# Kernel optimization log

Hardware: AMD Instinct MI355X
Metric: run time of the kernel (lower is better)

The kernel has to match this reference:

```python
import jax, jax.numpy as jnp
import numpy as np
import math

NUM_HEADS = 12
POS_BND = 16                 # patch_num
RPE_NUM = 2 * POS_BND + 1    # 33
LOGIT_SCALE_MAX = math.log(1.0 / 0.01)
EPS_NORM = 1e-12


def setup_inputs() -> dict:
    key = jax.random.key(0)
    ks = jax.random.split(key, 8)
    L, N, C = 257, 32, 768   # L = 16*16 patches + 1 CLS
    H, W = 16, 16
    x = jax.random.normal(ks[0], (L, N, C), dtype=jnp.float32)
    depth = jax.random.uniform(ks[1], (N, 1, H, W), dtype=jnp.float32)
    in_proj_w = jax.random.normal(ks[2], (3 * C, C), dtype=jnp.float32) * 0.02
    in_proj_b = jnp.zeros((3 * C,), dtype=jnp.float32)
    out_proj_w = jax.random.normal(ks[3], (C, C), dtype=jnp.float32) * 0.02
    out_proj_b = jnp.zeros((C,), dtype=jnp.float32)
    rpe_table = jax.random.normal(ks[4], (3 * RPE_NUM, NUM_HEADS), dtype=jnp.float32) * 0.02
    logit_scale = jnp.log(10.0) * jnp.ones((NUM_HEADS, 1, 1), dtype=jnp.float32)
    return {
        "x": x, "depth": depth,
        "in_proj_w": in_proj_w, "in_proj_b": in_proj_b,
        "out_proj_w": out_proj_w, "out_proj_b": out_proj_b,
        "rpe_table": rpe_table, "logit_scale": logit_scale,
    }


def _rpe_bias(depth, rpe_table):
    # depth: (B, 1, H, W) -> bias (B*num_heads, H*W, H*W)
    d = depth[:, 0]                              # (B, H, W)
    B, H, W = d.shape
    ii, jj = jnp.meshgrid(jnp.arange(H), jnp.arange(W), indexing="ij")
    xg = (jj.astype(jnp.float32) / (W - 1))[None].repeat(B, axis=0)   # (B,H,W)
    yg = (ii.astype(jnp.float32) / (H - 1))[None].repeat(B, axis=0)
    z_min = d.min(axis=(-2, -1), keepdims=True)
    z_max = d.max(axis=(-2, -1), keepdims=True)
    z = (d - z_min) / (z_max - z_min + 1e-8)
    coords = jnp.stack([xg, yg, z], axis=-1).reshape(B, H * W, 3)     # (B,HW,3)
    rel = coords[:, :, None, :] - coords[:, None, :, :]               # (B,HW,HW,3)
    idx = jnp.clip(jnp.round(rel * POS_BND).astype(jnp.int32), -POS_BND, POS_BND)
    idx = idx + POS_BND + jnp.arange(3, dtype=jnp.int32) * RPE_NUM    # (B,HW,HW,3)
    bias = rpe_table[idx].sum(axis=3)                                 # (B,HW,HW,heads)
    bias = bias.transpose(0, 3, 1, 2)                                 # (B,heads,HW,HW)
    return bias.reshape(-1, H * W, H * W)


def reference(x, depth, in_proj_w, in_proj_b, out_proj_w, out_proj_b, rpe_table, logit_scale):
    L, N, C = x.shape
    Hn = NUM_HEADS
    hd = C // Hn
    qkv = x @ in_proj_w.T + in_proj_b                     # (L,N,3C)
    q, k, v = jnp.split(qkv, 3, axis=-1)
    def to_heads(t):
        return t.reshape(L, N * Hn, hd).transpose(1, 0, 2)  # (N*Hn, L, hd)
    q, k, v = to_heads(q), to_heads(k), to_heads(v)
    # scaled-cosine attention: normalized q,k then clamped exp(log-scale)
    qn = q / jnp.maximum(jnp.linalg.norm(q, axis=-1, keepdims=True), EPS_NORM)
    kn = k / jnp.maximum(jnp.linalg.norm(k, axis=-1, keepdims=True), EPS_NORM)
    attn = jnp.einsum("bld,bmd->blm", qn, kn)             # (N*Hn, L, L)
    scale = jnp.exp(jnp.minimum(logit_scale, LOGIT_SCALE_MAX))   # (Hn,1,1)
    attn = (attn.reshape(N, Hn, L, L) * scale).reshape(N * Hn, L, L)
    # relative-position bias on patch tokens (skip CLS at index 0)
    res = _rpe_bias(depth, rpe_table)                     # (N*Hn, L-1, L-1)
    attn = attn.at[:, 1:, 1:].add(res)
    attn = jax.nn.softmax(attn, axis=-1)
    out = jnp.einsum("blm,bmd->bld", attn, v)             # (N*Hn, L, hd)
    out = out.transpose(1, 0, 2).reshape(L, N, C)
    out = out @ out_proj_w.T + out_proj_b
    return out, attn
```

## Files before the change

kernel.cpp:

```cpp
#include <hip/hip_runtime.h>
#include <math.h>

#define L_TOK 257
#define N_B 32
#define C_DIM 768
#define N_H 12
#define HD 64
#define BH (N_B * N_H)
#define M_TOK (L_TOK * N_B)
#define HW 256
#define RPE_NUM 33
#define LOGIT_MAX 4.6051701859880913680f
#define VT_STRIDE 264
#define MT_Q 65
#define NT_Q 18
#define NT_O 6
#define NTK 24

typedef unsigned short ushort;
typedef unsigned int uint;
typedef __attribute__((ext_vector_type(8))) short short8;
typedef __attribute__((ext_vector_type(4))) float f32x4;

__device__ __forceinline__ ushort f2bf_rn(float f) {
  uint u = __float_as_uint(f);
  uint r = (u + 0x7FFF + ((u >> 16) & 1)) >> 16;
  return (ushort)r;
}
__device__ __forceinline__ float bf2f(ushort h) {
  return __uint_as_float(((uint)h) << 16);
}

__device__ __forceinline__ int xcd_swz(int wid, int nwg) {
  int q = nwg >> 3, r = nwg & 7;
  int xcd = wid & 7, pos = wid >> 3;
  int base = (xcd < r) ? xcd * (q + 1) : r * (q + 1) + (xcd - r) * q;
  return base + pos;
}

__device__ __forceinline__ void tile_map(int bid, int MT, int NT, int nwg,
                                         int& m0, int& nt) {
  int wid = xcd_swz(bid, nwg);
  int per = 8 * NT;
  int s = wid / per;
  int rem = wid - s * per;
  int msz = MT - s * 8; if (msz > 8) msz = 8;
  int mi = rem % msz, ni = rem / msz;
  m0 = (s * 8 + mi) * 128;
  nt = ni;
}

__global__ __launch_bounds__(256)
void cvt_split(const float* __restrict__ src, ushort* __restrict__ hi,
               ushort* __restrict__ lo, int n) {
  int i = (blockIdx.x * 256 + threadIdx.x) * 4;
  if (i + 3 >= n + 3) return;
  if (i + 3 < n) {
    float4 v = *(const float4*)(src + i);
    ushort h0 = f2bf_rn(v.x), h1 = f2bf_rn(v.y), h2 = f2bf_rn(v.z), h3 = f2bf_rn(v.w);
    ushort l0 = f2bf_rn(v.x - bf2f(h0)), l1 = f2bf_rn(v.y - bf2f(h1));
    ushort l2 = f2bf_rn(v.z - bf2f(h2)), l3 = f2bf_rn(v.w - bf2f(h3));
    *(ushort4*)(hi + i) = make_ushort4(h0, h1, h2, h3);
    *(ushort4*)(lo + i) = make_ushort4(l0, l1, l2, l3);
  } else {
    for (int k = i; k < n; ++k) {
      float vv = src[k];
      ushort h = f2bf_rn(vv);
      hi[k] = h; lo[k] = f2bf_rn(vv - bf2f(h));
    }
  }
}

__device__ __forceinline__ void stage_pair(const ushort* g0, const ushort* g1,
                                           ushort* l, uint so) {
  __builtin_amdgcn_global_load_lds(
      (const __attribute__((address_space(1))) void*)g0,
      (__attribute__((address_space(3))) void*)((char*)l + so), 16, 0, 0);
  __builtin_amdgcn_global_load_lds(
      (const __attribute__((address_space(1))) void*)g1,
      (__attribute__((address_space(3))) void*)((char*)l + so + 4096), 16, 0, 0);
}

#define PH_WAIT(N)                                        \
  asm volatile("s_waitcnt vmcnt(" #N ")" ::: "memory");   \
  __builtin_amdgcn_s_barrier();                           \
  __builtin_amdgcn_sched_barrier(0);

#define PH_LGKM()                                         \
  asm volatile("s_waitcnt lgkmcnt(0)" ::: "memory");      \
  __builtin_amdgcn_sched_barrier(0);

__device__ __forceinline__ void gemm3_core(
    const ushort* __restrict__ Ahi, const ushort* __restrict__ Alo,
    const ushort* __restrict__ Bhi, const ushort* __restrict__ Blo,
    int m0, int n0, ushort* lds, f32x4 (&acc)[4][4]) {
  const int K = C_DIM, M = M_TOK;
  const int t = threadIdx.x;
  const int wave = t >> 6, lane = t & 63;
  const int wm = (wave & 1) * 64, wn = (wave >> 1) * 64;
  const int frm = lane & 15, fs = lane >> 4;
  const int sx = (fs ^ ((frm >> 1) & 3)) * 8;

  const int ar = t >> 2;
  const int acs = ((t & 3) ^ ((ar >> 1) & 3)) * 8;
  const uint so = (uint)(t & 192) * 16;

  int rA0 = m0 + ar;      if (rA0 > M - 1) rA0 = M - 1;
  int rA1 = m0 + 64 + ar; if (rA1 > M - 1) rA1 = M - 1;
  const size_t gA0 = (size_t)rA0 * K + acs;
  const size_t gA1 = (size_t)rA1 * K + acs;
  const size_t gB0 = (size_t)(n0 + ar) * K + acs;
  const size_t gB1 = (size_t)(n0 + 64 + ar) * K + acs;

  stage_pair(Ahi + gA0, Ahi + gA1, lds, so);
  stage_pair(Bhi + gB0, Bhi + gB1, lds + 4096, so);
  stage_pair(Alo + gA0, Alo + gA1, lds + 8192, so);
  stage_pair(Blo + gB0, Blo + gB1, lds + 12288, so);

  short8 ah[4], bh[4], al[4], bl[4];

#pragma unroll 2
  for (int kt = 0; kt < NTK - 1; ++kt) {
    const int curo = (kt & 1) << 14;
    const int nxo = curo ^ 16384;
    const int kn = (kt + 1) * 32;
    PH_WAIT(4)
#pragma unroll
    for (int i = 0; i < 4; ++i) {
      ah[i] = *(const short8*)(lds + curo + (wm + i * 16 + frm) * 32 + sx);
      bh[i] = *(const short8*)(lds + curo + 4096 + (wn + i * 16 + frm) * 32 + sx);
    }
    stage_pair(Ahi + gA0 + kn, Ahi + gA1 + kn, lds + nxo, so);
    stage_pair(Bhi + gB0 + kn, Bhi + gB1 + kn, lds + nxo + 4096, so);
    PH_LGKM()
    __builtin_amdgcn_s_setprio(1);
#pragma unroll
    for (int i = 0; i < 4; ++i)
#pragma unroll
      for (int j = 0; j < 4; ++j)
        acc[i][j] = __builtin_amdgcn_mfma_f32_16x16x32_bf16(ah[i], bh[j], acc[i][j], 0, 0, 0);
    __builtin_amdgcn_s_setprio(0);
    __builtin_amdgcn_sched_barrier(0);
    PH_WAIT(4)
#pragma unroll
    for (int i = 0; i < 4; ++i) {
      al[i] = *(const short8*)(lds + curo + 8192 + (wm + i * 16 + frm) * 32 + sx);
      bl[i] = *(const short8*)(lds + curo + 12288 + (wn + i * 16 + frm) * 32 + sx);
    }
    stage_pair(Alo + gA0 + kn, Alo + gA1 + kn, lds + nxo + 8192, so);
    stage_pair(Blo + gB0 + kn, Blo + gB1 + kn, lds + nxo + 12288, so);
    PH_LGKM()
    __builtin_amdgcn_s_setprio(1);
#pragma unroll
    for (int i = 0; i < 4; ++i)
#pragma unroll
      for (int j = 0; j < 4; ++j)
        acc[i][j] = __builtin_amdgcn_mfma_f32_16x16x32_bf16(al[i], bh[j], acc[i][j], 0, 0, 0);
#pragma unroll
    for (int i = 0; i < 4; ++i)
#pragma unroll
      for (int j = 0; j < 4; ++j)
        acc[i][j] = __builtin_amdgcn_mfma_f32_16x16x32_bf16(ah[i], bl[j], acc[i][j], 0, 0, 0);
    __builtin_amdgcn_s_setprio(0);
    __builtin_amdgcn_sched_barrier(0);
  }
  {
    const int curo = ((NTK - 1) & 1) << 14;
    PH_WAIT(4)
#pragma unroll
    for (int i = 0; i < 4; ++i) {
      ah[i] = *(const short8*)(lds + curo + (wm + i * 16 + frm) * 32 + sx);
      bh[i] = *(const short8*)(lds + curo + 4096 + (wn + i * 16 + frm) * 32 + sx);
    }
    PH_LGKM()
#pragma unroll
    for (int i = 0; i < 4; ++i)
#pragma unroll
      for (int j = 0; j < 4; ++j)
        acc[i][j] = __builtin_amdgcn_mfma_f32_16x16x32_bf16(ah[i], bh[j], acc[i][j], 0, 0, 0);
    __builtin_amdgcn_sched_barrier(0);
    PH_WAIT(0)
#pragma unroll
    for (int i = 0; i < 4; ++i) {
      al[i] = *(const short8*)(lds + curo + 8192 + (wm + i * 16 + frm) * 32 + sx);
      bl[i] = *(const short8*)(lds + curo + 12288 + (wn + i * 16 + frm) * 32 + sx);
    }
    PH_LGKM()
#pragma unroll
    for (int i = 0; i < 4; ++i)
#pragma unroll
      for (int j = 0; j < 4; ++j)
        acc[i][j] = __builtin_amdgcn_mfma_f32_16x16x32_bf16(al[i], bh[j], acc[i][j], 0, 0, 0);
#pragma unroll
    for (int i = 0; i < 4; ++i)
#pragma unroll
      for (int j = 0; j < 4; ++j)
        acc[i][j] = __builtin_amdgcn_mfma_f32_16x16x32_bf16(ah[i], bl[j], acc[i][j], 0, 0, 0);
    __builtin_amdgcn_sched_barrier(0);
  }
}

__global__ __launch_bounds__(256, 2)
void gemm_qkv_fused(const ushort* __restrict__ Ahi, const ushort* __restrict__ Alo,
                    const ushort* __restrict__ Bhi, const ushort* __restrict__ Blo,
                    const float* __restrict__ bias,
                    ushort* __restrict__ qhi, ushort* __restrict__ qlo,
                    ushort* __restrict__ khi, ushort* __restrict__ klo,
                    float* __restrict__ vout) {
  __shared__ __align__(16) ushort lds[32768];
  int m0, nt;
  tile_map(blockIdx.x, MT_Q, NT_Q, MT_Q * NT_Q, m0, nt);
  const int n0 = nt * 128;
  f32x4 acc[4][4] = {};
  gemm3_core(Ahi, Alo, Bhi, Blo, m0, n0, lds, acc);

  const int M = M_TOK;
  const int t = threadIdx.x;
  const int wave = t >> 6, lane = t & 63;
  const int wm = (wave & 1) * 64, wn = (wave >> 1) * 64;
  const int c0 = lane & 15, g = lane >> 4;
  const int colBase = n0 + wn;
  const int sect = colBase / C_DIM;
  const int hh = (colBase - sect * C_DIM) >> 6;
  float bv[4];
#pragma unroll
  for (int j = 0; j < 4; ++j) bv[j] = bias[colBase + j * 16 + c0];

#pragma unroll
  for (int i = 0; i < 4; ++i) {
#pragma unroll
    for (int r = 0; r < 4; ++r) {
      const int row = m0 + wm + i * 16 + g * 4 + r;
      float lv[4];
#pragma unroll
      for (int j = 0; j < 4; ++j) lv[j] = acc[i][j][r] + bv[j];
      if (sect == 2) {
        if (row < M) {
          int l = row >> 5, n = row & 31;
          size_t ob = ((size_t)((n * N_H + hh) * L_TOK + l)) * HD;
#pragma unroll
          for (int j = 0; j < 4; ++j) vout[ob + j * 16 + c0] = lv[j];
        }
      } else {
        float ss = lv[0] * lv[0] + lv[1] * lv[1] + lv[2] * lv[2] + lv[3] * lv[3];
        ss += __shfl_xor(ss, 1);
        ss += __shfl_xor(ss, 2);
        ss += __shfl_xor(ss, 4);
        ss += __shfl_xor(ss, 8);
        float inv = 1.0f / fmaxf(sqrtf(ss), 1e-12f);
        if (row < M) {
          int l = row >> 5, n = row & 31;
          size_t ob = ((size_t)((n * N_H + hh) * L_TOK + l)) * HD;
          ushort* dh = sect ? khi : qhi;
          ushort* dl = sect ? klo : qlo;
#pragma unroll
          for (int j = 0; j < 4; ++j) {
            float val = lv[j] * inv;
            ushort hv = f2bf_rn(val);
            dh[ob + j * 16 + c0] = hv;
            dl[ob + j * 16 + c0] = f2bf_rn(val - bf2f(hv));
          }
        }
      }
    }
  }
}

__global__ __launch_bounds__(256, 2)
void gemm_out(const ushort* __restrict__ Ahi, const ushort* __restrict__ Alo,
              const ushort* __restrict__ Bhi, const ushort* __restrict__ Blo,
              const float* __restrict__ bias, float* __restrict__ Cout) {
  __shared__ __align__(16) ushort lds[32768];
  int m0, nt;
  tile_map(blockIdx.x, MT_Q, NT_O, MT_Q * NT_O, m0, nt);
  const int n0 = nt * 128;
  f32x4 acc[4][4] = {};
  gemm3_core(Ahi, Alo, Bhi, Blo, m0, n0, lds, acc);

  const int M = M_TOK, Nn = C_DIM;
  const int t = threadIdx.x;
  const int wave = t >> 6, lane = t & 63;
  const int wm = (wave & 1) * 64, wn = (wave >> 1) * 64;
  const int ecol = lane & 15;
#pragma unroll
  for (int j = 0; j < 4; ++j) {
    int col = n0 + wn + j * 16 + ecol;
    float bv = bias[col];
#pragma unroll
    for (int i = 0; i < 4; ++i) {
      int rbase = m0 + wm + i * 16 + (lane >> 4) * 4;
#pragma unroll
      for (int r = 0; r < 4; ++r) {
        int row = rbase + r;
        if (row < M) Cout[(size_t)row * Nn + col] = acc[i][j][r] + bv;
      }
    }
  }
}

__global__ __launch_bounds__(256)
void vt_make(const float* __restrict__ v, ushort* __restrict__ vthi,
             ushort* __restrict__ vtlo) {
  __shared__ float sT[64][65];
  const int b = blockIdx.x;
  const int t = threadIdx.x;
  const float* vb = v + (size_t)b * L_TOK * HD;
  ushort* vh = vthi + (size_t)b * HD * VT_STRIDE;
  ushort* vl = vtlo + (size_t)b * HD * VT_STRIDE;
  for (int k0 = 0; k0 < 256; k0 += 64) {
#pragma unroll
    for (int p = 0; p < 16; ++p) {
      int idx = p * 256 + t;
      int k = idx >> 6, d = idx & 63;
      sT[d][k] = vb[(size_t)(k0 + k) * HD + d];
    }
    __syncthreads();
#pragma unroll
    for (int p = 0; p < 16; ++p) {
      int idx = p * 256 + t;
      int d = idx >> 6, k = idx & 63;
      float val = sT[d][k];
      ushort h = f2bf_rn(val);
      vh[(size_t)d * VT_STRIDE + k0 + k] = h;
      vl[(size_t)d * VT_STRIDE + k0 + k] = f2bf_rn(val - bf2f(h));
    }
    __syncthreads();
  }
  if (t < HD) {
    float val = vb[(size_t)256 * HD + t];
    ushort h = f2bf_rn(val);
    vh[(size_t)t * VT_STRIDE + 256] = h;
    vl[(size_t)t * VT_STRIDE + 256] = f2bf_rn(val - bf2f(h));
  }
}

__global__ __launch_bounds__(256)
void attn_mfma(const ushort* __restrict__ qhi, const ushort* __restrict__ qlo,
               const ushort* __restrict__ khi, const ushort* __restrict__ klo,
               const float* __restrict__ depth, const float* __restrict__ rpe,
               const float* __restrict__ lscale, float* __restrict__ P) {
  __shared__ __align__(16) ushort sKh[256 * 72];
  __shared__ __align__(16) ushort sKl[256 * 72];
  __shared__ float cz_s[HW];
  __shared__ float txd[32], tyd[32], tzt[36];
  __shared__ float red_s[16];
  __shared__ float s256[4][16];
  __shared__ float qs[HD];
  __shared__ float lg6_sh;

  const int tile = blockIdx.x;
  const int b = blockIdx.y;
  const int n = b / N_H, h = b - n * N_H;
  const int t = threadIdx.x;
  const int lane = t & 63, wave = t >> 6;

  float dval = depth[n * HW + t];
  float mn = dval, mx = dval;
#pragma unroll
  for (int o = 32; o > 0; o >>= 1) {
    mn = fminf(mn, __shfl_down(mn, o));
    mx = fmaxf(mx, __shfl_down(mx, o));
  }
  if (lane == 0) { red_s[wave] = mn; red_s[8 + wave] = mx; }
  __syncthreads();
  float zmin = fminf(fminf(red_s[0], red_s[1]), fminf(red_s[2], red_s[3]));
  float zmax = fmaxf(fmaxf(red_s[8], red_s[9]), fmaxf(red_s[10], red_s[11]));
  float den = zmax - zmin + 1e-8f;
  cz_s[t] = (dval - zmin) / den;
  if (t < 31) {
    int d = t - 15;
    int ix = (int)rintf((float)d * (16.0f / 15.0f));
    ix = max(-16, min(16, ix));
    txd[t] = rpe[(ix + 16) * N_H + h];
    tyd[t] = rpe[(RPE_NUM + ix + 16) * N_H + h];
  }
  if (t < RPE_NUM) tzt[t] = rpe[(2 * RPE_NUM + t) * N_H + h];
  const float scale = expf(fminf(lscale[h], LOGIT_MAX));

  const ushort* khb = khi + (size_t)b * L_TOK * HD;
  const ushort* klb = klo + (size_t)b * L_TOK * HD;
#pragma unroll
  for (int it = 0; it < 8; ++it) {
    int idx = it * 256 + t;
    int j = idx >> 3, c = (idx & 7) * 8;
    *(uint4*)(sKh + j * 72 + c) = *(const uint4*)(khb + (size_t)j * HD + c);
    *(uint4*)(sKl + j * 72 + c) = *(const uint4*)(klb + (size_t)j * HD + c);
  }
  __syncthreads();

  const int qrow = tile * 64 + 16 * wave;
  const size_t qoff = ((size_t)b * L_TOK + qrow + (lane & 15)) * HD + (lane >> 4) * 8;
  short8 qh0 = *(const short8*)(qhi + qoff);
  short8 qh1 = *(const short8*)(qhi + qoff + 32);
  short8 ql0 = *(const short8*)(qlo + qoff);
  short8 ql1 = *(const short8*)(qlo + qoff + 32);

  f32x4 acc[16] = {};
#pragma unroll
  for (int jt = 0; jt < 16; ++jt) {
    const ushort* bp = sKh + (jt * 16 + (lane & 15)) * 72 + (lane >> 4) * 8;
    const ushort* bq = sKl + (jt * 16 + (lane & 15)) * 72 + (lane >> 4) * 8;
    short8 bh0 = *(const short8*)(bp);
    short8 bh1 = *(const short8*)(bp + 32);
    short8 bl0 = *(const short8*)(bq);
    short8 bl1 = *(const short8*)(bq + 32);
    acc[jt] = __builtin_amdgcn_mfma_f32_16x16x32_bf16(qh0, bh0, acc[jt], 0, 0, 0);
    acc[jt] = __builtin_amdgcn_mfma_f32_16x16x32_bf16(qh1, bh1, acc[jt], 0, 0, 0);
    acc[jt] = __builtin_amdgcn_mfma_f32_16x16x32_bf16(qh0, bl0, acc[jt], 0, 0, 0);
    acc[jt] = __builtin_amdgcn_mfma_f32_16x16x32_bf16(qh1, bl1, acc[jt], 0, 0, 0);
    acc[jt] = __builtin_amdgcn_mfma_f32_16x16x32_bf16(ql0, bh0, acc[jt], 0, 0, 0);
    acc[jt] = __builtin_amdgcn_mfma_f32_16x16x32_bf16(ql1, bh1, acc[jt], 0, 0, 0);
  }

  {
    const ushort* k6h = khb + (size_t)256 * HD + (lane >> 4) * 8;
    const ushort* k6l = klb + (size_t)256 * HD + (lane >> 4) * 8;
    float p = 0.f;
#pragma unroll
    for (int j = 0; j < 8; ++j) {
      float kf0 = bf2f(k6h[j]) + bf2f(k6l[j]);
      float kf1 = bf2f(k6h[32 + j]) + bf2f(k6l[32 + j]);
      float qf0 = bf2f((ushort)qh0[j]) + bf2f((ushort)ql0[j]);
      float qf1 = bf2f((ushort)qh1[j]) + bf2f((ushort)ql1[j]);
      p = fmaf(qf0, kf0, fmaf(qf1, kf1, p));
    }
    p += __shfl_xor(p, 16);
    p += __shfl_xor(p, 32);
    if (lane < 16) s256[wave][lane] = p;
  }

  const int g = lane >> 4, c0 = lane & 15;

  float lg6[4];
#pragma unroll
  for (int r = 0; r < 4; ++r) {
    int gi = tile * 64 + 16 * wave + 4 * g + r;
    float d6 = s256[wave][4 * g + r];
    float bz = 0.f;
    if (gi >= 1) {
      int dx = ((gi - 1) & 15) - 15;
      int dy = ((gi - 1) >> 4) - 15;
      float rz = (cz_s[gi - 1] - cz_s[255]) * 16.0f;
      int iz = (int)rintf(rz); iz = max(-16, min(16, iz));
      bz = txd[dx + 15] + tyd[dy + 15] + tzt[iz + 16];
    }
    lg6[r] = scale * d6 + bz;
  }

#pragma unroll
  for (int jt = 0; jt < 16; ++jt) {
    int col = jt * 16 + c0;
#pragma unroll
    for (int r = 0; r < 4; ++r) {
      int gi = tile * 64 + 16 * wave + 4 * g + r;
      float lv = scale * acc[jt][r];
      if (col >= 1 && gi >= 1) {
        int dx = ((gi - 1) & 15) - ((col - 1) & 15);
        int dy = ((gi - 1) >> 4) - ((col - 1) >> 4);
        float rz = (cz_s[gi - 1] - cz_s[col - 1]) * 16.0f;
        int iz = (int)rintf(rz); iz = max(-16, min(16, iz));
        lv += txd[dx + 15] + tyd[dy + 15] + tzt[iz + 16];
      }
      acc[jt][r] = lv;
    }
  }

  float* Pb_ = P + (size_t)b * L_TOK * L_TOK;
#pragma unroll
  for (int r = 0; r < 4; ++r) {
    int gi = tile * 64 + 16 * wave + 4 * g + r;
    float m = acc[0][r];
#pragma unroll
    for (int jt = 1; jt < 16; ++jt) m = fmaxf(m, acc[jt][r]);
#pragma unroll
    for (int o = 1; o < 16; o <<= 1) m = fmaxf(m, __shfl_xor(m, o));
    m = fmaxf(m, lg6[r]);
    float s = 0.f;
#pragma unroll
    for (int jt = 0; jt < 16; ++jt) {
      float e = __expf(acc[jt][r] - m);
      acc[jt][r] = e;
      s += e;
    }
#pragma unroll
    for (int o = 1; o < 16; o <<= 1) s += __shfl_xor(s, o);
    float e6 = __expf(lg6[r] - m);
    float inv = 1.0f / (s + e6);
    float* Prow = Pb_ + (size_t)gi * L_TOK;
#pragma unroll
    for (int jt = 0; jt < 16; ++jt)
      Prow[jt * 16 + c0] = acc[jt][r] * inv;
    if (c0 == 0) Prow[256] = e6 * inv;
  }

  if (tile == 0) {
    __syncthreads();
    const size_t q6 = ((size_t)b * L_TOK + 256) * HD;
    if (t < HD) qs[t] = bf2f(qhi[q6 + t]) + bf2f(qlo[q6 + t]);
    __syncthreads();

    const ushort* krh = sKh + t * 72;
    const ushort* krl = sKl + t * 72;
    float dot = 0.f;
#pragma unroll
    for (int c = 0; c < HD; c += 8) {
      ushort4 hv0 = *(const ushort4*)(krh + c);
      ushort4 hv1 = *(const ushort4*)(krh + c + 4);
      ushort4 lv0 = *(const ushort4*)(krl + c);
      ushort4 lv1 = *(const ushort4*)(krl + c + 4);
      dot = fmaf(bf2f(hv0.x) + bf2f(lv0.x), qs[c + 0], dot);
      dot = fmaf(bf2f(hv0.y) + bf2f(lv0.y), qs[c + 1], dot);
      dot = fmaf(bf2f(hv0.z) + bf2f(lv0.z), qs[c + 2], dot);
      dot = fmaf(bf2f(hv0.w) + bf2f(lv0.w), qs[c + 3], dot);
      dot = fmaf(bf2f(hv1.x) + bf2f(lv1.x), qs[c + 4], dot);
      dot = fmaf(bf2f(hv1.y) + bf2f(lv1.y), qs[c + 5], dot);
      dot = fmaf(bf2f(hv1.z) + bf2f(lv1.z), qs[c + 6], dot);
      dot = fmaf(bf2f(hv1.w) + bf2f(lv1.w), qs[c + 7], dot);
    }

    float lg;
    {
      float bsum = 0.f;
      if (t >= 1) {
        int dx = 15 - ((t - 1) & 15);
        int dy = 15 - ((t - 1) >> 4);
        float rz = (cz_s[255] - cz_s[t - 1]) * 16.0f;
        int iz = (int)rintf(rz); iz = max(-16, min(16, iz));
        bsum = txd[dx + 15] + tyd[dy + 15] + tzt[iz + 16];
      }
      lg = scale * dot + bsum;
    }

    if (wave == 0) {
      const ushort* k6h = khi + q6;
      const ushort* k6l = klo + q6;
      float pp = (bf2f(k6h[lane]) + bf2f(k6l[lane])) * qs[lane];
#pragma unroll
      for (int o = 32; o > 0; o >>= 1) pp += __shfl_down(pp, o);
      if (lane == 0) {
        float bz = txd[15] + tyd[15] + tzt[16];
        lg6_sh = scale * pp + bz;
      }
    }

    float m = lg;
#pragma unroll
    for (int o = 32; o > 0; o >>= 1) m = fmaxf(m, __shfl_down(m, o));
    if (lane == 0) red_s[wave] = m;
    __syncthreads();
    float M = fmaxf(fmaxf(red_s[0], red_s[1]), fmaxf(red_s[2], red_s[3]));
    M = fmaxf(M, lg6_sh);
    float e = __expf(lg - M);
    float s = e;
#pragma unroll
    for (int o = 32; o > 0; o >>= 1) s += __shfl_down(s, o);
    if (lane == 0) red_s[8 + wave] = s;
    __syncthreads();
    float e6 = __expf(lg6_sh - M);
    float S = (red_s[8] + red_s[9]) + (red_s[10] + red_s[11]) + e6;
    float inv = 1.0f / S;
    float* Prow = Pb_ + (size_t)256 * L_TOK;
    Prow[t] = e * inv;
    if (t == 0) Prow[256] = e6 * inv;
  }
}

__global__ __launch_bounds__(256)
void pv_mfma(const float* __restrict__ P, const ushort* __restrict__ vthi,
             const ushort* __restrict__ vtlo, const float* __restrict__ v,
             ushort* __restrict__ ahi, ushort* __restrict__ alo) {
  const int b = blockIdx.y;
  const int n = b / N_H, h = b - n * N_H;
  const int t = threadIdx.x;
  const int lane = t & 63, wave = t >> 6;
  const int rbase = blockIdx.x * 128 + wave * 32;
  const float* Pb = P + (size_t)b * L_TOK * L_TOK;
  const ushort* vh = vthi + (size_t)b * HD * VT_STRIDE;
  const ushort* vl = vtlo + (size_t)b * HD * VT_STRIDE;

  const int fm = lane & 15, fk = (lane >> 4) * 8;
  f32x4 acc[2][4] = {};

  for (int k0 = 0; k0 < 256; k0 += 32) {
    short8 ah[2], al[2], bh[4], bl[4];
#pragma unroll
    for (int i = 0; i < 2; ++i) {
      const float* pr = Pb + (size_t)(rbase + i * 16 + fm) * L_TOK + k0 + fk;
#pragma unroll
      for (int j = 0; j < 8; ++j) {
        float pv_ = pr[j];
        ushort hh = f2bf_rn(pv_);
        ah[i][j] = (short)hh;
        al[i][j] = (short)f2bf_rn(pv_ - bf2f(hh));
      }
    }
#pragma unroll
    for (int j = 0; j < 4; ++j) {
      const ushort* bp = vh + (size_t)(j * 16 + fm) * VT_STRIDE + k0 + fk;
      const ushort* bq = vl + (size_t)(j * 16 + fm) * VT_STRIDE + k0 + fk;
      bh[j] = *(const short8*)bp;
      bl[j] = *(const short8*)bq;
    }
#pragma unroll
    for (int i = 0; i < 2; ++i)
#pragma unroll
      for (int j = 0; j < 4; ++j) {
        acc[i][j] = __builtin_amdgcn_mfma_f32_16x16x32_bf16(ah[i], bh[j], acc[i][j], 0, 0, 0);
        acc[i][j] = __builtin_amdgcn_mfma_f32_16x16x32_bf16(ah[i], bl[j], acc[i][j], 0, 0, 0);
        acc[i][j] = __builtin_amdgcn_mfma_f32_16x16x32_bf16(al[i], bh[j], acc[i][j], 0, 0, 0);
        acc[i][j] = __builtin_amdgcn_mfma_f32_16x16x32_bf16(al[i], bl[j], acc[i][j], 0, 0, 0);
      }
  }

  const int g = lane >> 4;
  float v6[4];
#pragma unroll
  for (int j = 0; j < 4; ++j)
    v6[j] = v[((size_t)b * L_TOK + 256) * HD + j * 16 + fm];
#pragma unroll
  for (int i = 0; i < 2; ++i)
#pragma unroll
    for (int r = 0; r < 4; ++r) {
      int row = rbase + i * 16 + g * 4 + r;
      float p6 = Pb[(size_t)row * L_TOK + 256];
#pragma unroll
      for (int j = 0; j < 4; ++j) acc[i][j][r] += p6 * v6[j];
    }

#pragma unroll
  for (int i = 0; i < 2; ++i)
#pragma unroll
    for (int r = 0; r < 4; ++r) {
      int row = rbase + i * 16 + g * 4 + r;
      size_t o = ((size_t)row * N_B + n) * C_DIM + h * HD;
#pragma unroll
      for (int j = 0; j < 4; ++j) {
        float val = acc[i][j][r];
        ushort hv = f2bf_rn(val);
        ahi[o + j * 16 + fm] = hv;
        alo[o + j * 16 + fm] = f2bf_rn(val - bf2f(hv));
      }
    }

  if (blockIdx.x == 0 && t < HD) {
    const float* Prow = Pb + (size_t)256 * L_TOK;
    const float* vb = v + (size_t)b * L_TOK * HD;
    float sum = 0.f;
    for (int k = 0; k < L_TOK; ++k)
      sum = fmaf(Prow[k], vb[(size_t)k * HD + t], sum);
    size_t o = ((size_t)256 * N_B + n) * C_DIM + h * HD + t;
    ushort hv = f2bf_rn(sum);
    ahi[o] = hv;
    alo[o] = f2bf_rn(sum - bf2f(hv));
  }
}

extern "C" void kernel_launch(void* const* d_in, const int* in_sizes, int n_in,
                              void* d_out, int out_size, void* d_ws, size_t ws_size,
                              hipStream_t stream) {
  const float* x      = (const float*)d_in[0];
  const float* depth  = (const float*)d_in[1];
  const float* w_in   = (const float*)d_in[2];
  const float* b_in   = (const float*)d_in[3];
  const float* w_out  = (const float*)d_in[4];
  const float* b_out  = (const float*)d_in[5];
  const float* rpe    = (const float*)d_in[6];
  const float* lscale = (const float*)d_in[7];
  float* out = (float*)d_out;
  float* ws = (float*)d_ws;

  ushort* xhi  = (ushort*)ws;
  ushort* xlo  = xhi + 6316032;
  ushort* vthi = (ushort*)(ws + 6316032);
  ushort* vtlo = vthi + 6488064;
  float*  v    = ws + 18948096;
  ushort* qhi  = (ushort*)(ws + 25264128);
  ushort* qlo  = qhi + 6316032;
  ushort* khi  = qlo + 6316032;
  ushort* klo  = khi + 6316032;
  ushort* wihi = (ushort*)(ws + 37896192);
  ushort* wilo = wihi + 1769472;
  ushort* wohi = wilo + 1769472;
  ushort* wolo = wohi + 589824;
  ushort* ahi  = xhi;
  ushort* alo  = xlo;
  float* Pout = out + 6316032;

  cvt_split<<<6168, 256, 0, stream>>>(x, xhi, xlo, 6316032);
  cvt_split<<<1728, 256, 0, stream>>>(w_in, wihi, wilo, 1769472);
  cvt_split<<<576, 256, 0, stream>>>(w_out, wohi, wolo, 589824);

  gemm_qkv_fused<<<MT_Q * NT_Q, 256, 0, stream>>>(xhi, xlo, wihi, wilo, b_in,
                                                  qhi, qlo, khi, klo, v);
  vt_make<<<BH, 256, 0, stream>>>(v, vthi, vtlo);
  attn_mfma<<<dim3(4, BH), 256, 0, stream>>>(qhi, qlo, khi, klo, depth, rpe, lscale, Pout);
  pv_mfma<<<dim3(2, BH), 256, 0, stream>>>(Pout, vthi, vtlo, v, ahi, alo);

  gemm_out<<<MT_Q * NT_O, 256, 0, stream>>>(ahi, alo, wohi, wolo, b_out, out);
}
```

Measured before the change: 445.9 us.

## Fuse PV matmul into attention kernel using LDS-staged split-bf16 probabilities

Merges the separate pv_mfma kernel into the attention kernel. Each block writes its normalized probability tile as hi/lo bf16 pairs into shared memory, reusing the K buffer, then multiplies it against V^T with MFMA. This avoids re-reading the full fp32 probability matrix from global memory and removes one kernel launch. In exchange it adds a barrier, extra LDS writes and V loads per attention block, and the CLS-row path now reads K from global memory.

```diff
diff --git a/kernel.cpp b/kernel.cpp
--- a/kernel.cpp
+++ b/kernel.cpp
@@ -16,6 +16,7 @@
 #define NT_Q 18
 #define NT_O 6
 #define NTK 24
+#define P_STRIDE 264
 
 typedef unsigned short ushort;
 typedef unsigned int uint;
@@ -335,18 +336,26 @@
 }
 
 __global__ __launch_bounds__(256)
-void attn_mfma(const ushort* __restrict__ qhi, const ushort* __restrict__ qlo,
-               const ushort* __restrict__ khi, const ushort* __restrict__ klo,
-               const float* __restrict__ depth, const float* __restrict__ rpe,
-               const float* __restrict__ lscale, float* __restrict__ P) {
-  __shared__ __align__(16) ushort sKh[256 * 72];
-  __shared__ __align__(16) ushort sKl[256 * 72];
+void attn_pv(const ushort* __restrict__ qhi, const ushort* __restrict__ qlo,
+             const ushort* __restrict__ khi, const ushort* __restrict__ klo,
+             const ushort* __restrict__ vthi, const ushort* __restrict__ vtlo,
+             const float* __restrict__ v,
+             const float* __restrict__ depth, const float* __restrict__ rpe,
+             const float* __restrict__ lscale, float* __restrict__ P,
+             ushort* __restrict__ ahi, ushort* __restrict__ alo) {
+  __shared__ __align__(16) ushort sK[2 * 256 * 72];
   __shared__ float cz_s[HW];
   __shared__ float txd[32], tyd[32], tzt[36];
   __shared__ float red_s[16];
   __shared__ float s256[4][16];
   __shared__ float qs[HD];
   __shared__ float lg6_sh;
+  __shared__ float prow_s[257];
+
+  ushort* sKh = sK;
+  ushort* sKl = sK + 256 * 72;
+  ushort* Psh = sK;
+  ushort* Psl = sK + 64 * P_STRIDE;
 
   const int tile = blockIdx.x;
   const int b = blockIdx.y;
@@ -429,6 +438,8 @@
     if (lane < 16) s256[wave][lane] = p;
   }
 
+  __syncthreads();
+
   const int g = lane >> 4, c0 = lane & 15;
 
   float lg6[4];
@@ -466,9 +477,11 @@
   }
 
   float* Pb_ = P + (size_t)b * L_TOK * L_TOK;
+  float p6v[4];
 #pragma unroll
   for (int r = 0; r < 4; ++r) {
     int gi = tile * 64 + 16 * wave + 4 * g + r;
+    int lrw = 16 * wave + 4 * g + r;
     float m = acc[0][r];
 #pragma unroll
     for (int jt = 1; jt < 16; ++jt) m = fmaxf(m, acc[jt][r]);
@@ -486,21 +499,67 @@
     for (int o = 1; o < 16; o <<= 1) s += __shfl_xor(s, o);
     float e6 = __expf(lg6[r] - m);
     float inv = 1.0f / (s + e6);
+    p6v[r] = e6 * inv;
     float* Prow = Pb_ + (size_t)gi * L_TOK;
 #pragma unroll
-    for (int jt = 0; jt < 16; ++jt)
-      Prow[jt * 16 + c0] = acc[jt][r] * inv;
-    if (c0 == 0) Prow[256] = e6 * inv;
+    for (int jt = 0; jt < 16; ++jt) {
+      float pv_ = acc[jt][r] * inv;
+      Prow[jt * 16 + c0] = pv_;
+      ushort hv = f2bf_rn(pv_);
+      Psh[lrw * P_STRIDE + jt * 16 + c0] = hv;
+      Psl[lrw * P_STRIDE + jt * 16 + c0] = f2bf_rn(pv_ - bf2f(hv));
+    }
+    if (c0 == 0) Prow[256] = p6v[r];
+  }
+
+  const int fm = c0, fk = g * 8;
+  const ushort* vhb = vthi + (size_t)b * HD * VT_STRIDE;
+  const ushort* vlb = vtlo + (size_t)b * HD * VT_STRIDE;
+  const int lrow = 16 * wave + fm;
+  f32x4 pacc[4] = {};
+#pragma unroll
+  for (int k0 = 0; k0 < 256; k0 += 32) {
+    short8 pah = *(const short8*)(Psh + lrow * P_STRIDE + k0 + fk);
+    short8 pal = *(const short8*)(Psl + lrow * P_STRIDE + k0 + fk);
+#pragma unroll
+    for (int j = 0; j < 4; ++j) {
+      short8 vbh = *(const short8*)(vhb + (size_t)(j * 16 + fm) * VT_STRIDE + k0 + fk);
+      short8 vbl = *(const short8*)(vlb + (size_t)(j * 16 + fm) * VT_STRIDE + k0 + fk);
+      pacc[j] = __builtin_amdgcn_mfma_f32_16x16x32_bf16(pah, vbh, pacc[j], 0, 0, 0);
+      pacc[j] = __builtin_amdgcn_mfma_f32_16x16x32_bf16(pah, vbl, pacc[j], 0, 0, 0);
+      pacc[j] = __builtin_amdgcn_mfma_f32_16x16x32_bf16(pal, vbh, pacc[j], 0, 0, 0);
+      pacc[j] = __builtin_amdgcn_mfma_f32_16x16x32_bf16(pal, vbl, pacc[j], 0, 0, 0);
+    }
+  }
+  float v6[4];
+#pragma unroll
+  for (int j = 0; j < 4; ++j)
+    v6[j] = v[((size_t)b * L_TOK + 256) * HD + j * 16 + fm];
+#pragma unroll
+  for (int r = 0; r < 4; ++r)
+#pragma unroll
+    for (int j = 0; j < 4; ++j) pacc[j][r] += p6v[r] * v6[j];
+
+#pragma unroll
+  for (int r = 0; r < 4; ++r) {
+    int row = tile * 64 + 16 * wave + 4 * g + r;
+    size_t o = ((size_t)row * N_B + n) * C_DIM + h * HD;
+#pragma unroll
+    for (int j = 0; j < 4; ++j) {
+      float val = pacc[j][r];
+      ushort hv = f2bf_rn(val);
+      ahi[o + j * 16 + fm] = hv;
+      alo[o + j * 16 + fm] = f2bf_rn(val - bf2f(hv));
+    }
   }
 
   if (tile == 0) {
-    __syncthreads();
     const size_t q6 = ((size_t)b * L_TOK + 256) * HD;
     if (t < HD) qs[t] = bf2f(qhi[q6 + t]) + bf2f(qlo[q6 + t]);
     __syncthreads();
 
-    const ushort* krh = sKh + t * 72;
-    const ushort* krl = sKl + t * 72;
+    const ushort* krh = khb + (size_t)t * HD;
+    const ushort* krl = klb + (size_t)t * HD;
     float dot = 0.f;
 #pragma unroll
     for (int c = 0; c < HD; c += 8) {
@@ -560,98 +619,22 @@
     float S = (red_s[8] + red_s[9]) + (red_s[10] + red_s[11]) + e6;
     float inv = 1.0f / S;
     float* Prow = Pb_ + (size_t)256 * L_TOK;
-    Prow[t] = e * inv;
-    if (t == 0) Prow[256] = e6 * inv;
-  }
-}
-
-__global__ __launch_bounds__(256)
-void pv_mfma(const float* __restrict__ P, const ushort* __restrict__ vthi,
-             const ushort* __restrict__ vtlo, const float* __restrict__ v,
-             ushort* __restrict__ ahi, ushort* __restrict__ alo) {
-  const int b = blockIdx.y;
-  const int n = b / N_H, h = b - n * N_H;
-  const int t = threadIdx.x;
-  const int lane = t & 63, wave = t >> 6;
-  const int rbase = blockIdx.x * 128 + wave * 32;
-  const float* Pb = P + (size_t)b * L_TOK * L_TOK;
-  const ushort* vh = vthi + (size_t)b * HD * VT_STRIDE;
-  const ushort* vl = vtlo + (size_t)b * HD * VT_STRIDE;
-
-  const int fm = lane & 15, fk = (lane >> 4) * 8;
-  f32x4 acc[2][4] = {};
-
-  for (int k0 = 0; k0 < 256; k0 += 32) {
-    short8 ah[2], al[2], bh[4], bl[4];
-#pragma unroll
-    for (int i = 0; i < 2; ++i) {
-      const float* pr = Pb + (size_t)(rbase + i * 16 + fm) * L_TOK + k0 + fk;
-#pragma unroll
-      for (int j = 0; j < 8; ++j) {
-        float pv_ = pr[j];
-        ushort hh = f2bf_rn(pv_);
-        ah[i][j] = (short)hh;
-        al[i][j] = (short)f2bf_rn(pv_ - bf2f(hh));
-      }
-    }
-#pragma unroll
-    for (int j = 0; j < 4; ++j) {
-      const ushort* bp = vh + (size_t)(j * 16 + fm) * VT_STRIDE + k0 + fk;
-      const ushort* bq = vl + (size_t)(j * 16 + fm) * VT_STRIDE + k0 + fk;
-      bh[j] = *(const short8*)bp;
-      bl[j] = *(const short8*)bq;
-    }
-#pragma unroll
-    for (int i = 0; i < 2; ++i)
-#pragma unroll
-      for (int j = 0; j < 4; ++j) {
-        acc[i][j] = __builtin_amdgcn_mfma_f32_16x16x32_bf16(ah[i], bh[j], acc[i][j], 0, 0, 0);
-        acc[i][j] = __builtin_amdgcn_mfma_f32_16x16x32_bf16(ah[i], bl[j], acc[i][j], 0, 0, 0);
-        acc[i][j] = __builtin_amdgcn_mfma_f32_16x16x32_bf16(al[i], bh[j], acc[i][j], 0, 0, 0);
-        acc[i][j] = __builtin_amdgcn_mfma_f32_16x16x32_bf16(al[i], bl[j], acc[i][j], 0, 0, 0);
-      }
-  }
-
-  const int g = lane >> 4;
-  float v6[4];
-#pragma unroll
-  for (int j = 0; j < 4; ++j)
-    v6[j] = v[((size_t)b * L_TOK + 256) * HD + j * 16 + fm];
-#pragma unroll
-  for (int i = 0; i < 2; ++i)
-#pragma unroll
-    for (int r = 0; r < 4; ++r) {
-      int row = rbase + i * 16 + g * 4 + r;
-      float p6 = Pb[(size_t)row * L_TOK + 256];
-#pragma unroll
-      for (int j = 0; j < 4; ++j) acc[i][j][r] += p6 * v6[j];
-    }
-
-#pragma unroll
-  for (int i = 0; i < 2; ++i)
-#pragma unroll
-    for (int r = 0; r < 4; ++r) {
-      int row = rbase + i * 16 + g * 4 + r;
-      size_t o = ((size_t)row * N_B + n) * C_DIM + h * HD;
-#pragma unroll
-      for (int j = 0; j < 4; ++j) {
-        float val = acc[i][j][r];
-        ushort hv = f2bf_rn(val);
-        ahi[o + j * 16 + fm] = hv;
-        alo[o + j * 16 + fm] = f2bf_rn(val - bf2f(hv));
-      }
-    }
-
-  if (blockIdx.x == 0 && t < HD) {
-    const float* Prow = Pb + (size_t)256 * L_TOK;
-    const float* vb = v + (size_t)b * L_TOK * HD;
-    float sum = 0.f;
-    for (int k = 0; k < L_TOK; ++k)
-      sum = fmaf(Prow[k], vb[(size_t)k * HD + t], sum);
-    size_t o = ((size_t)256 * N_B + n) * C_DIM + h * HD + t;
-    ushort hv = f2bf_rn(sum);
-    ahi[o] = hv;
-    alo[o] = f2bf_rn(sum - bf2f(hv));
+    float pe = e * inv;
+    Prow[t] = pe;
+    prow_s[t] = pe;
+    if (t == 0) { Prow[256] = e6 * inv; prow_s[256] = e6 * inv; }
+    __syncthreads();
+
+    if (t < HD) {
+      const float* vb = v + (size_t)b * L_TOK * HD;
+      float sum = 0.f;
+      for (int k = 0; k < L_TOK; ++k)
+        sum = fmaf(prow_s[k], vb[(size_t)k * HD + t], sum);
+      size_t o = ((size_t)256 * N_B + n) * C_DIM + h * HD + t;
+      ushort hv = f2bf_rn(sum);
+      ahi[o] = hv;
+      alo[o] = f2bf_rn(sum - bf2f(hv));
+    }
   }
 }
 
@@ -693,8 +676,8 @@
   gemm_qkv_fused<<<MT_Q * NT_Q, 256, 0, stream>>>(xhi, xlo, wihi, wilo, b_in,
                                                   qhi, qlo, khi, klo, v);
   vt_make<<<BH, 256, 0, stream>>>(v, vthi, vtlo);
-  attn_mfma<<<dim3(4, BH), 256, 0, stream>>>(qhi, qlo, khi, klo, depth, rpe, lscale, Pout);
-  pv_mfma<<<dim3(2, BH), 256, 0, stream>>>(Pout, vthi, vtlo, v, ahi, alo);
+  attn_pv<<<dim3(4, BH), 256, 0, stream>>>(qhi, qlo, khi, klo, vthi, vtlo, v,
+                                           depth, rpe, lscale, Pout, ahi, alo);
 
   gemm_out<<<MT_Q * NT_O, 256, 0, stream>>>(ahi, alo, wohi, wolo, b_out, out);
 }
```

Measured after the change: 596.8 us. +33.8%, slower.
